# Optimization experiments

Hardware: AMD Instinct MI355X
Metric: run time of the kernel (lower is better)

## Reference

```python
import jax, jax.numpy as jnp
import numpy as np

B, T, C, H = 2, 2048, 1024, 16
HS = C // H        # head dim = 64
HALF = HS // 2     # rope half = 32


def _rope_cos_sin():
    # standard RoPE frequencies over the half-dim
    inv_freq = 1.0 / (10000.0 ** (np.arange(HALF, dtype=np.float32) / HALF))
    t = np.arange(T, dtype=np.float32)
    ang = np.outer(t, inv_freq)  # [T, HALF]
    cos = np.cos(ang)[None, None]  # [1,1,T,HALF]
    sin = np.sin(ang)[None, None]
    return jnp.asarray(cos), jnp.asarray(sin)


def setup_inputs() -> dict:
    key = jax.random.key(0)
    k1, k2, k3 = jax.random.split(key, 3)
    cos, sin = _rope_cos_sin()
    return {
        "x": jax.random.normal(k1, (B, T, C), dtype=jnp.float32),
        "cos": cos,
        "sin": sin,
        "w_attn": jax.random.normal(k2, (C, 3 * C), dtype=jnp.float32) * (1.0 / np.sqrt(C)),
        "b_attn": jnp.zeros((3 * C,), dtype=jnp.float32),
        "w_proj": jax.random.normal(k3, (C, C), dtype=jnp.float32) * (1.0 / np.sqrt(C)),
        "b_proj": jnp.zeros((C,), dtype=jnp.float32),
    }


def _rope_apply(x, cos, sin):
    # x: [B,H,T,HS]; cos/sin: [1,1,T,HALF]
    x1, x2 = x[..., :HALF], x[..., HALF:]
    return jnp.concatenate([x1 * cos - x2 * sin, x1 * sin + x2 * cos], axis=-1)


def reference(x, cos, sin, w_attn, b_attn, w_proj, b_proj):
    b, t, c = x.shape
    qkv = x @ w_attn + b_attn                      # [B,T,3C]
    q, k, v = jnp.split(qkv, 3, axis=-1)
    # [B,T,C] -> [B,H,T,HS]
    def to_heads(u):
        return u.reshape(b, t, H, HS).transpose(0, 2, 1, 3)
    q, k, v = to_heads(q), to_heads(k), to_heads(v)
    q = _rope_apply(q, cos[:, :, :t], sin[:, :, :t])
    k = _rope_apply(k, cos[:, :, :t], sin[:, :, :t])
    scale = 1.0 / np.sqrt(HS).astype(np.float32)
    scores = jnp.einsum("bhqd,bhkd->bhqk", q, k) * scale
    causal = jnp.tril(jnp.ones((t, t), dtype=bool))
    scores = jnp.where(causal, scores, jnp.finfo(scores.dtype).min)
    attn = jax.nn.softmax(scores, axis=-1)
    ctx = jnp.einsum("bhqk,bhkd->bhqd", attn, v)   # [B,H,T,HS]
    ctx = ctx.transpose(0, 2, 1, 3).reshape(b, t, c)
    return ctx @ w_proj + b_proj
```

## Files before the change

kernel.cpp:

```cpp
#include <hip/hip_runtime.h>
#include <hip/hip_bf16.h>

#define Bn    2
#define Tdim  2048
#define Cdim  1024
#define Hn    16
#define HSd   64
#define Mrows 4096

typedef unsigned short u16;
typedef __attribute__((ext_vector_type(8))) short short8;
typedef __attribute__((ext_vector_type(4))) float f32x4;

__device__ __forceinline__ u16 f2bf(float f) {
  union { __hip_bfloat16 h; u16 u; } cv;
  cv.h = __float2bfloat16(f);
  return cv.u;
}

#define GLOAD_LDS16(g, l)                                                     \
  __builtin_amdgcn_global_load_lds(                                           \
      (const __attribute__((address_space(1))) void*)(g),                     \
      (__attribute__((address_space(3))) void*)(l), 16, 0, 0)

#define CFENCE asm volatile("" ::: "memory")

__global__ __launch_bounds__(256) void k_prep(const float* __restrict__ x,
                                              u16* __restrict__ xb,
                                              const float* __restrict__ wattn,
                                              u16* __restrict__ wattnT,
                                              const float* __restrict__ wproj,
                                              u16* __restrict__ wprojT) {
  __shared__ float tile[64][65];
  const int bid = blockIdx.x, tid = threadIdx.x;
  if (bid < 4096) {
    int i = bid * 256 + tid;
    float4 v = ((const float4*)x)[i];
    unsigned o0 = (unsigned)f2bf(v.x) | ((unsigned)f2bf(v.y) << 16);
    unsigned o1 = (unsigned)f2bf(v.z) | ((unsigned)f2bf(v.w) << 16);
    ((uint2*)xb)[i] = make_uint2(o0, o1);
    return;
  }
  const float* in;
  u16* out;
  int Cc, c0, r0;
  if (bid < 4096 + 768) {
    int b = bid - 4096;
    in = wattn; out = wattnT; Cc = 3072;
    c0 = (b % 48) * 64; r0 = (b / 48) * 64;
  } else {
    int b = bid - 4864;
    in = wproj; out = wprojT; Cc = 1024;
    c0 = (b % 16) * 64; r0 = (b / 16) * 64;
  }
  const int R = 1024;
  int lc = tid & 63, l0 = tid >> 6;
  for (int rr = l0; rr < 64; rr += 4)
    tile[rr][lc] = in[(size_t)(r0 + rr) * Cc + c0 + lc];
  __syncthreads();
  for (int rr = l0; rr < 64; rr += 4)
    out[(size_t)(c0 + rr) * R + r0 + lc] = f2bf(tile[lc][rr]);
}

__global__ __launch_bounds__(256) void k_transpose_v(const u16* __restrict__ Vh,
                                                     u16* __restrict__ Vt) {
  __shared__ u16 tile[64][72];
  int bh = blockIdx.y, t0 = blockIdx.x * 64;
  int lc = threadIdx.x & 63, l0 = threadIdx.x >> 6;
  const u16* src = Vh + (size_t)bh * Tdim * HSd;
  u16* dst = Vt + (size_t)bh * HSd * Tdim;
  for (int rr = l0; rr < 64; rr += 4)
    tile[rr][lc] = src[(size_t)(t0 + rr) * HSd + lc];
  __syncthreads();
  for (int dd = l0; dd < 64; dd += 4)
    dst[(size_t)dd * Tdim + t0 + lc] = tile[lc][dd];
}

template <int EPI, int BM, int BN, int WM, int WN>
__global__ __launch_bounds__(64 * WM * WN, 4) void k_gemm2(
    const u16* __restrict__ A, const u16* __restrict__ Bt,
    const float* __restrict__ bias, const float* __restrict__ cosT,
    const float* __restrict__ sinT, u16* __restrict__ Qh, u16* __restrict__ Kh,
    u16* __restrict__ Vh, float* __restrict__ Out, int Ndim, int Kdim) {
  __shared__ u16 As[2][BM * 32];
  __shared__ u16 Bs[2][BN * 32];
  const int tid = threadIdx.x;
  const int wid = tid >> 6, lane = tid & 63;
  const int wr = wid / WN, wc = wid % WN;
  const int lr = lane & 15, lg = lane >> 4;
  const int m0 = blockIdx.x * BM, n0 = blockIdx.y * BN;
  const int wm = wr * 64, wn = wc * 64;

  f32x4 acc[4][4] = {};

  const u16* Ag = A + (size_t)m0 * Kdim;
  const u16* Bg = Bt + (size_t)n0 * Kdim;
  const int srw = lane >> 2;
  const int scb = ((lane & 3) ^ ((lane >> 3) & 3)) << 4;
  constexpr int NW = WM * WN;
  constexpr int CPW = (BM + BN) / 16 / NW;
  constexpr int CA = BM / 16;

#define STAGE2(bi, t)                                                         \
  do {                                                                        \
    _Pragma("unroll") for (int cc = 0; cc < CPW; ++cc) {                      \
      int c = wid * CPW + cc;                                                 \
      if (c < CA)                                                             \
        GLOAD_LDS16(                                                          \
            (const char*)(Ag + (size_t)(c * 16 + srw) * Kdim + (t)*32) + scb, \
            As[bi] + c * 512);                                                \
      else                                                                    \
        GLOAD_LDS16((const char*)(Bg + (size_t)((c - CA) * 16 + srw) * Kdim + \
                                  (t)*32) +                                   \
                        scb,                                                  \
                    Bs[bi] + (c - CA) * 512);                                 \
    }                                                                         \
  } while (0)

#define LDFRAG(buf, row)                                                      \
  (*(const short8*)((const char*)(buf) + (row)*64 +                           \
                    ((lg * 16) ^ ((((row) >> 1) & 3) << 4))))

  const int nt = Kdim >> 5;
  STAGE2(0, 0);
  asm volatile("s_waitcnt vmcnt(0)" ::: "memory");
  __builtin_amdgcn_s_barrier();
  CFENCE;

  int cur = 0;
  for (int t = 0; t < nt; ++t) {
    if (t + 1 < nt) STAGE2(cur ^ 1, t + 1);
    const u16* ab = As[cur];
    const u16* bb = Bs[cur];
    short8 a[4], b[4];
#pragma unroll
    for (int i = 0; i < 4; ++i) a[i] = LDFRAG(ab, wm + i * 16 + lr);
#pragma unroll
    for (int j = 0; j < 4; ++j) b[j] = LDFRAG(bb, wn + j * 16 + lr);
    asm volatile("s_waitcnt lgkmcnt(0)" ::: "memory");
    __builtin_amdgcn_sched_barrier(0);
    __builtin_amdgcn_s_setprio(1);
#pragma unroll
    for (int i = 0; i < 4; ++i)
#pragma unroll
      for (int j = 0; j < 4; ++j)
        acc[i][j] =
            __builtin_amdgcn_mfma_f32_16x16x32_bf16(a[i], b[j], acc[i][j], 0, 0, 0);
    __builtin_amdgcn_s_setprio(0);
    CFENCE;
    asm volatile("s_waitcnt vmcnt(0)" ::: "memory");
    __builtin_amdgcn_s_barrier();
    CFENCE;
    cur ^= 1;
  }
#undef STAGE2
#undef LDFRAG

  const int nbase = n0 + wn;
  if (EPI == 0) {
    const int sec = nbase >> 10;
    const int hh = (nbase & 1023) >> 6;
    const float qs = (sec == 0) ? 0.125f : 1.0f;
    float bj[4];
#pragma unroll
    for (int nj = 0; nj < 4; ++nj) bj[nj] = bias[nbase + nj * 16 + lr];
#pragma unroll
    for (int mi = 0; mi < 4; ++mi) {
      int growb = m0 + wm + mi * 16 + 4 * lg;
#pragma unroll
      for (int r = 0; r < 4; ++r) {
        int gr = growb + r;
        int bI = gr >> 11, tq = gr & (Tdim - 1);
        size_t off = ((size_t)(bI * Hn + hh) * Tdim + tq) * HSd;
        if (sec < 2) {
          u16* dst = (sec == 0) ? Qh : Kh;
#pragma unroll
          for (int nj = 0; nj < 2; ++nj) {
            int d = nj * 16 + lr;
            float v1 = acc[mi][nj][r] + bj[nj];
            float v2 = acc[mi][nj + 2][r] + bj[nj + 2];
            float cs = cosT[tq * 32 + d], sn = sinT[tq * 32 + d];
            dst[off + d] = f2bf((v1 * cs - v2 * sn) * qs);
            dst[off + d + 32] = f2bf((v1 * sn + v2 * cs) * qs);
          }
        } else {
#pragma unroll
          for (int nj = 0; nj < 4; ++nj)
            Vh[off + nj * 16 + lr] = f2bf(acc[mi][nj][r] + bj[nj]);
        }
      }
    }
  } else {
#pragma unroll
    for (int mi = 0; mi < 4; ++mi) {
      int growb = m0 + wm + mi * 16 + 4 * lg;
#pragma unroll
      for (int r = 0; r < 4; ++r) {
        int gr = growb + r;
#pragma unroll
        for (int nj = 0; nj < 4; ++nj) {
          int col = nbase + nj * 16 + lr;
          Out[(size_t)gr * Ndim + col] = acc[mi][nj][r] + bias[col];
        }
      }
    }
  }
}

__global__ __launch_bounds__(512, 4) void k_attn(const u16* __restrict__ Qh,
                                                 const u16* __restrict__ Kh,
                                                 const u16* __restrict__ Vt,
                                                 u16* __restrict__ ctx) {
  __shared__ u16 Ks[2][64 * 64];
  __shared__ u16 Vs[2][64 * 64];
  __shared__ u16 Plds[8][16][72];
  const int tid = threadIdx.x;
  const int wid = tid >> 6, lane = tid & 63;
  const int lr = lane & 15, lg = lane >> 4;
  const int bid = blockIdx.x;
  const int xb = 15 - (bid >> 5);
  const int bh = bid & 31;
  const int qr0 = xb * 128 + wid * 16;
  const int nt = 2 * xb + 2;
  const int itd = qr0 >> 6;
  const u16* Q = Qh + (size_t)bh * Tdim * HSd;
  const u16* K = Kh + (size_t)bh * Tdim * HSd;
  const u16* V = Vt + (size_t)bh * HSd * Tdim;

  short8 qf0 = *(const short8*)(Q + (size_t)(qr0 + lr) * HSd + 8 * lg);
  short8 qf1 = *(const short8*)(Q + (size_t)(qr0 + lr) * HSd + 32 + 8 * lg);

  const int srow = lane >> 3;
  const int scol = 16 * ((lane & 7) ^ srow);
  const int swz = (lr & 7) << 4;

  f32x4 ctxa[4] = {};
  float ssum[4] = {0.f, 0.f, 0.f, 0.f};
  const float L2E = 1.44269504089f;
  const float MC = 24.0f * L2E;
  const f32x4 zero = {};

#define STAGE_KV(b, kv0)                                                      \
  do {                                                                        \
    GLOAD_LDS16((const char*)(K + (size_t)((kv0) + wid * 8 + srow) * HSd) +   \
                    scol,                                                     \
                Ks[b] + wid * 8 * 64);                                        \
    GLOAD_LDS16((const char*)(V + (size_t)(wid * 8 + srow) * Tdim + (kv0)) +  \
                    scol,                                                     \
                Vs[b] + wid * 8 * 64);                                        \
  } while (0)

  STAGE_KV(0, 0);
  __syncthreads();

  int cur = 0;
  for (int it = 0; it < nt; ++it) {
    const int kv0 = it * 64;
    if (it + 1 < nt) STAGE_KV(cur ^ 1, kv0 + 64);

    if (it <= itd) {
      const char* ksb = (const char*)(Ks[cur]);
      const char* vsb = (const char*)(Vs[cur]);

      f32x4 s[4];
#pragma unroll
      for (int f = 0; f < 4; ++f) {
        int row = 16 * f + lr;
        int c0 = (lg * 16) ^ swz;
        short8 kf0 = *(const short8*)(ksb + row * 128 + c0);
        short8 kf1 = *(const short8*)(ksb + row * 128 + (c0 ^ 64));
        s[f] = __builtin_amdgcn_mfma_f32_16x16x32_bf16(qf0, kf0, zero, 0, 0, 0);
        s[f] = __builtin_amdgcn_mfma_f32_16x16x32_bf16(qf1, kf1, s[f], 0, 0, 0);
      }

#pragma unroll
      for (int r = 0; r < 4; ++r) {
        if (it == itd) {
          int q = qr0 + 4 * lg + r;
#pragma unroll
          for (int f = 0; f < 4; ++f)
            if (kv0 + 16 * f + lr > q) s[f][r] = -1e30f;
        }
#pragma unroll
        for (int f = 0; f < 4; ++f) {
          float p = __builtin_amdgcn_exp2f(fmaf(s[f][r], L2E, -MC));
          ssum[r] += p;
          Plds[wid][4 * lg + r][16 * f + lr] = f2bf(p);
        }
      }

      const char* pb = (const char*)(&Plds[wid][0][0]);
      short8 pa0 = *(const short8*)(pb + lr * 144 + lg * 16);
      short8 pa1 = *(const short8*)(pb + lr * 144 + 64 + lg * 16);

#pragma unroll
      for (int dt = 0; dt < 4; ++dt) {
        int row = 16 * dt + lr;
        int c0 = (lg * 16) ^ swz;
        short8 vb0 = *(const short8*)(vsb + row * 128 + c0);
        short8 vb1 = *(const short8*)(vsb + row * 128 + (c0 ^ 64));
        ctxa[dt] =
            __builtin_amdgcn_mfma_f32_16x16x32_bf16(pa0, vb0, ctxa[dt], 0, 0, 0);
        ctxa[dt] =
            __builtin_amdgcn_mfma_f32_16x16x32_bf16(pa1, vb1, ctxa[dt], 0, 0, 0);
      }
    }

    __syncthreads();
    cur ^= 1;
  }
#undef STAGE_KV

  const int bI = bh >> 4, hh = bh & 15;
#pragma unroll
  for (int r = 0; r < 4; ++r) {
    float s = ssum[r];
    s += __shfl_xor(s, 1);
    s += __shfl_xor(s, 2);
    s += __shfl_xor(s, 4);
    s += __shfl_xor(s, 8);
    float inv = 1.0f / s;
    int t = qr0 + 4 * lg + r;
    size_t off = ((size_t)bI * Tdim + t) * Cdim + hh * HSd;
#pragma unroll
    for (int dt = 0; dt < 4; dt++)
      ctx[off + dt * 16 + lr] = f2bf(ctxa[dt][r] * inv);
  }
}

extern "C" void kernel_launch(void* const* d_in, const int* in_sizes, int n_in,
                              void* d_out, int out_size, void* d_ws,
                              size_t ws_size, hipStream_t stream) {
  const float* x = (const float*)d_in[0];
  const float* cosT = (const float*)d_in[1];
  const float* sinT = (const float*)d_in[2];
  const float* wattn = (const float*)d_in[3];
  const float* battn = (const float*)d_in[4];
  const float* wproj = (const float*)d_in[5];
  const float* bproj = (const float*)d_in[6];
  float* out = (float*)d_out;
  char* ws = (char*)d_ws;
  const size_t MB = 1024 * 1024;
  u16* xb = (u16*)(ws + 0);
  u16* Vt = (u16*)(ws + 0);
  u16* wattnT = (u16*)(ws + 8 * MB);
  u16* wprojT = (u16*)(ws + 14 * MB);
  u16* Qh = (u16*)(ws + 16 * MB);
  u16* Kh = (u16*)(ws + 24 * MB);
  u16* Vh = (u16*)(ws + 32 * MB);
  u16* ctx = (u16*)(ws + 40 * MB);

  k_prep<<<5120, 256, 0, stream>>>(x, xb, wattn, wattnT, wproj, wprojT);
  k_gemm2<0, 128, 256, 2, 4><<<dim3(32, 12), 512, 0, stream>>>(
      xb, wattnT, battn, cosT, sinT, Qh, Kh, Vh, nullptr, 3072, 1024);
  k_transpose_v<<<dim3(32, 32), 256, 0, stream>>>(Vh, Vt);
  k_attn<<<512, 512, 0, stream>>>(Qh, Kh, Vt, ctx);
  k_gemm2<1, 128, 128, 2, 2><<<dim3(32, 8), 256, 0, stream>>>(
      ctx, wprojT, bproj, nullptr, nullptr, nullptr, nullptr, nullptr, out,
      1024, 1024);
}
```

Measured before the change: 201.0 us.

## Triple-buffer GEMM LDS staging with partial vmcnt waits

Both GEMMs move from double- to triple-buffered LDS staging. Global-to-LDS loads are issued two k-tiles ahead, and the loop waits only for the older tile with a partial vmcnt count instead of draining every outstanding load. The explicit lgkmcnt wait and sched_barrier before the MFMAs are dropped, and the min-waves launch bound becomes a template parameter (3 for the projection GEMM). This is meant to hide global memory latency better, at the cost of more LDS per block, which can lower occupancy.

```diff
diff --git a/kernel.cpp b/kernel.cpp
--- a/kernel.cpp
+++ b/kernel.cpp
@@ -76,14 +76,16 @@
     dst[(size_t)dd * Tdim + t0 + lc] = tile[lc][dd];
 }
 
-template <int EPI, int BM, int BN, int WM, int WN>
-__global__ __launch_bounds__(64 * WM * WN, 4) void k_gemm2(
+template <int EPI, int BM, int BN, int WM, int WN, int MINW>
+__global__ __launch_bounds__(64 * WM * WN, MINW) void k_gemm2(
     const u16* __restrict__ A, const u16* __restrict__ Bt,
     const float* __restrict__ bias, const float* __restrict__ cosT,
     const float* __restrict__ sinT, u16* __restrict__ Qh, u16* __restrict__ Kh,
     u16* __restrict__ Vh, float* __restrict__ Out, int Ndim, int Kdim) {
-  __shared__ u16 As[2][BM * 32];
-  __shared__ u16 Bs[2][BN * 32];
+  __shared__ u16 As[3][BM * 32];
+  __shared__ u16 Bs[3][BN * 32];
+  u16* const Asm = &As[0][0];
+  u16* const Bsm = &Bs[0][0];
   const int tid = threadIdx.x;
   const int wid = tid >> 6, lane = tid & 63;
   const int wr = wid / WN, wc = wid % WN;
@@ -100,21 +102,32 @@
   constexpr int NW = WM * WN;
   constexpr int CPW = (BM + BN) / 16 / NW;
   constexpr int CA = BM / 16;
+  static_assert(CPW == 3 || CPW == 4, "vmcnt literal table");
 
 #define STAGE2(bi, t)                                                         \
   do {                                                                        \
+    u16* aDst = Asm + (bi) * (BM * 32);                                       \
+    u16* bDst = Bsm + (bi) * (BN * 32);                                       \
     _Pragma("unroll") for (int cc = 0; cc < CPW; ++cc) {                      \
       int c = wid * CPW + cc;                                                 \
       if (c < CA)                                                             \
         GLOAD_LDS16(                                                          \
             (const char*)(Ag + (size_t)(c * 16 + srw) * Kdim + (t)*32) + scb, \
-            As[bi] + c * 512);                                                \
+            aDst + c * 512);                                                  \
       else                                                                    \
         GLOAD_LDS16((const char*)(Bg + (size_t)((c - CA) * 16 + srw) * Kdim + \
                                   (t)*32) +                                   \
                         scb,                                                  \
-                    Bs[bi] + (c - CA) * 512);                                 \
+                    bDst + (c - CA) * 512);                                   \
     }                                                                         \
+  } while (0)
+
+#define WAIT_CPW                                                              \
+  do {                                                                        \
+    if constexpr (CPW == 3)                                                   \
+      asm volatile("s_waitcnt vmcnt(3)" ::: "memory");                        \
+    else                                                                      \
+      asm volatile("s_waitcnt vmcnt(4)" ::: "memory");                        \
   } while (0)
 
 #define LDFRAG(buf, row)                                                      \
@@ -123,22 +136,24 @@
 
   const int nt = Kdim >> 5;
   STAGE2(0, 0);
-  asm volatile("s_waitcnt vmcnt(0)" ::: "memory");
+  STAGE2(1, 1);
+  WAIT_CPW;
   __builtin_amdgcn_s_barrier();
   CFENCE;
 
   int cur = 0;
   for (int t = 0; t < nt; ++t) {
-    if (t + 1 < nt) STAGE2(cur ^ 1, t + 1);
-    const u16* ab = As[cur];
-    const u16* bb = Bs[cur];
+    int st = cur + 2;
+    if (st >= 3) st -= 3;
+    if (t + 2 < nt) STAGE2(st, t + 2);
+    CFENCE;
+    const u16* ab = Asm + cur * (BM * 32);
+    const u16* bb = Bsm + cur * (BN * 32);
     short8 a[4], b[4];
 #pragma unroll
     for (int i = 0; i < 4; ++i) a[i] = LDFRAG(ab, wm + i * 16 + lr);
 #pragma unroll
     for (int j = 0; j < 4; ++j) b[j] = LDFRAG(bb, wn + j * 16 + lr);
-    asm volatile("s_waitcnt lgkmcnt(0)" ::: "memory");
-    __builtin_amdgcn_sched_barrier(0);
     __builtin_amdgcn_s_setprio(1);
 #pragma unroll
     for (int i = 0; i < 4; ++i)
@@ -148,12 +163,18 @@
             __builtin_amdgcn_mfma_f32_16x16x32_bf16(a[i], b[j], acc[i][j], 0, 0, 0);
     __builtin_amdgcn_s_setprio(0);
     CFENCE;
-    asm volatile("s_waitcnt vmcnt(0)" ::: "memory");
-    __builtin_amdgcn_s_barrier();
-    CFENCE;
-    cur ^= 1;
+    if (t + 2 < nt)
+      WAIT_CPW;
+    else if (t + 2 == nt)
+      asm volatile("s_waitcnt vmcnt(0)" ::: "memory");
+    if (t + 1 < nt) {
+      __builtin_amdgcn_s_barrier();
+      CFENCE;
+    }
+    cur = (cur == 2) ? 0 : cur + 1;
   }
 #undef STAGE2
+#undef WAIT_CPW
 #undef LDFRAG
 
   const int nbase = n0 + wn;
@@ -351,11 +372,11 @@
   u16* ctx = (u16*)(ws + 40 * MB);
 
   k_prep<<<5120, 256, 0, stream>>>(x, xb, wattn, wattnT, wproj, wprojT);
-  k_gemm2<0, 128, 256, 2, 4><<<dim3(32, 12), 512, 0, stream>>>(
+  k_gemm2<0, 128, 256, 2, 4, 4><<<dim3(32, 12), 512, 0, stream>>>(
       xb, wattnT, battn, cosT, sinT, Qh, Kh, Vh, nullptr, 3072, 1024);
   k_transpose_v<<<dim3(32, 32), 256, 0, stream>>>(Vh, Vt);
   k_attn<<<512, 512, 0, stream>>>(Qh, Kh, Vt, ctx);
-  k_gemm2<1, 128, 128, 2, 2><<<dim3(32, 8), 256, 0, stream>>>(
+  k_gemm2<1, 128, 128, 2, 2, 3><<<dim3(32, 8), 256, 0, stream>>>(
       ctx, wprojT, bproj, nullptr, nullptr, nullptr, nullptr, nullptr, out,
       1024, 1024);
 }
```

Result: no change. 202.2 us (+0.6%).
